# Kernel tuning notes

Measured on AMD Instinct MI355X. Metric: run time of the kernel, lower is better.

Reference implementation:

```python
import jax, jax.numpy as jnp
import numpy as np

B, T, C, H = 4, 1024, 1024, 16
D = C // H  # head dim = 64
EPS = 1e-5


def _layernorm(x, g, b):
    m = jnp.mean(x, axis=-1, keepdims=True)
    v = jnp.var(x, axis=-1, keepdims=True)
    return (x - m) / jnp.sqrt(v + EPS) * g + b


def setup_inputs() -> dict:
    key = jax.random.key(0)
    ks = jax.random.split(key, 8)
    s = 0.02  # GPT-style init scale
    w = lambda k, shp: (jax.random.normal(k, shp, jnp.float32) * s)
    return {
        "x": jax.random.normal(ks[0], (B, T, C), jnp.float32),
        "ln1_g": jnp.ones((C,), jnp.float32), "ln1_b": jnp.zeros((C,), jnp.float32),
        "wq": w(ks[1], (C, C)), "bq": jnp.zeros((C,), jnp.float32),
        "wk": w(ks[2], (C, C)), "bk": jnp.zeros((C,), jnp.float32),
        "wv": w(ks[3], (C, C)), "bv": jnp.zeros((C,), jnp.float32),
        "wo": w(ks[4], (C, C)), "bo": jnp.zeros((C,), jnp.float32),
        "ln2_g": jnp.ones((C,), jnp.float32), "ln2_b": jnp.zeros((C,), jnp.float32),
        "w1": w(ks[5], (C, 4 * C)), "b1": jnp.zeros((4 * C,), jnp.float32),
        "w2": w(ks[6], (4 * C, C)), "b2": jnp.zeros((C,), jnp.float32),
    }


def reference(x, ln1_g, ln1_b, wq, bq, wk, bk, wv, bv, wo, bo,
              ln2_g, ln2_b, w1, b1, w2, b2):
    # --- causal self-attention branch: x = x + attn(ln1(x)) ---
    h = _layernorm(x, ln1_g, ln1_b)
    q = (h @ wq + bq).reshape(B, T, H, D)
    k = (h @ wk + bk).reshape(B, T, H, D)
    v = (h @ wv + bv).reshape(B, T, H, D)
    att = jnp.einsum('bqhd,bkhd->bhqk', q, k) * (1.0 / np.sqrt(D).astype(np.float32))
    causal = jnp.tril(jnp.ones((T, T), bool))
    att = jnp.where(causal, att, -jnp.inf)
    att = jax.nn.softmax(att, axis=-1)  # dropout p=0 -> identity
    y = jnp.einsum('bhqk,bkhd->bqhd', att, v).reshape(B, T, C)
    x = x + (y @ wo + bo)
    # --- MLP branch: x = x + mlp(ln2(x)) ---
    h2 = _layernorm(x, ln2_g, ln2_b)
    m = jax.nn.gelu(h2 @ w1 + b1, approximate=False)  # torch nn.GELU default = exact erf
    x = x + (m @ w2 + b2)
    return x
```

## Files before the change

### kernel.cpp

```cpp
#include <hip/hip_runtime.h>
#include <hip/hip_bf16.h>
#include <math.h>

#define B_ 4
#define T_ 1024
#define C_ 1024
#define H_ 16
#define D_ 64
#define M_ (B_*T_)

typedef __bf16 bf16;
typedef __bf16 bf16x8 __attribute__((ext_vector_type(8)));
typedef float  f32x4  __attribute__((ext_vector_type(4)));

#define MFMA16(a, b, c) __builtin_amdgcn_mfma_f32_16x16x32_bf16((a), (b), (c), 0, 0, 0)

__device__ __forceinline__ void gload16(const void* g, void* l) {
  __builtin_amdgcn_global_load_lds((const __attribute__((address_space(1))) void*)g,
                                   (__attribute__((address_space(3))) void*)l,
                                   16, 0, 0);
}

__global__ __launch_bounds__(256) void wprep(const float* __restrict__ wq,
                                             const float* __restrict__ wk,
                                             const float* __restrict__ wv,
                                             const float* __restrict__ wo,
                                             const float* __restrict__ w1,
                                             const float* __restrict__ w2,
                                             bf16* __restrict__ WqkvT,
                                             bf16* __restrict__ WoT,
                                             bf16* __restrict__ W1T,
                                             bf16* __restrict__ W2T) {
  __shared__ float tile[32][33];
  const int b = blockIdx.x;
  const float* W; bf16* WT; int K, N, n0, k0;
  if (b < 3072)      { const int w = b >> 10, t = b & 1023;
                       W = (w == 0) ? wq : ((w == 1) ? wk : wv);
                       WT = WqkvT + (size_t)w * 1024 * 1024;
                       K = 1024; N = 1024; n0 = (t & 31) * 32; k0 = (t >> 5) * 32; }
  else if (b < 4096) { const int t = b - 3072; W = wo; WT = WoT;
                       K = 1024; N = 1024; n0 = (t & 31) * 32; k0 = (t >> 5) * 32; }
  else if (b < 8192) { const int t = b - 4096; W = w1; WT = W1T;
                       K = 1024; N = 4096; n0 = (t & 127) * 32; k0 = (t >> 7) * 32; }
  else               { const int t = b - 8192; W = w2; WT = W2T;
                       K = 4096; N = 1024; n0 = (t & 31) * 32; k0 = (t >> 5) * 32; }
  const int tx = threadIdx.x & 31, ty = threadIdx.x >> 5;
#pragma unroll
  for (int i = ty; i < 32; i += 8)
    tile[i][tx] = W[(size_t)(k0 + i) * N + n0 + tx];
  __syncthreads();
#pragma unroll
  for (int i = ty; i < 32; i += 8)
    WT[(size_t)(n0 + i) * K + k0 + tx] = (bf16)tile[tx][i];
}

__global__ __launch_bounds__(256) void bcat(const float* __restrict__ a,
                                            const float* __restrict__ b,
                                            const float* __restrict__ c,
                                            float* __restrict__ o) {
  int i = blockIdx.x * 256 + threadIdx.x;
  o[i] = (i < 1024) ? a[i] : ((i < 2048) ? b[i - 1024] : c[i - 2048]);
}

__global__ __launch_bounds__(256) void ln_k(const float* __restrict__ x,
                                            const float* __restrict__ g,
                                            const float* __restrict__ b,
                                            bf16* __restrict__ out) {
  int row = blockIdx.x;
  int t = threadIdx.x;
  float4 xv = ((const float4*)(x + (size_t)row * C_))[t];
  float s  = xv.x + xv.y + xv.z + xv.w;
  float ss = xv.x*xv.x + xv.y*xv.y + xv.z*xv.z + xv.w*xv.w;
#pragma unroll
  for (int m = 32; m; m >>= 1) { s += __shfl_xor(s, m); ss += __shfl_xor(ss, m); }
  __shared__ float red[8];
  int wid = t >> 6;
  if ((t & 63) == 0) { red[wid] = s; red[4 + wid] = ss; }
  __syncthreads();
  s  = red[0] + red[1] + red[2] + red[3];
  ss = red[4] + red[5] + red[6] + red[7];
  float mean = s * (1.0f / C_);
  float var  = ss * (1.0f / C_) - mean * mean;
  float inv  = rsqrtf(var + 1e-5f);
  float4 gv = ((const float4*)g)[t];
  float4 bv = ((const float4*)b)[t];
  bf16* o = out + (size_t)row * C_ + t * 4;
  o[0] = (bf16)((xv.x - mean) * inv * gv.x + bv.x);
  o[1] = (bf16)((xv.y - mean) * inv * gv.y + bv.y);
  o[2] = (bf16)((xv.z - mean) * inv * gv.z + bv.z);
  o[3] = (bf16)((xv.w - mean) * inv * gv.w + bv.w);
}

template <int BM, int BN, int WM, int WN, int EPI>
__global__ __launch_bounds__(WM*WN*64, 4)
void gemms(const bf16* __restrict__ A, const bf16* __restrict__ BT,
           const float* __restrict__ bias, const float* __restrict__ res,
           void* __restrict__ outp, int N, int K, int gx) {
  constexpr int NT = WM * WN * 64;
  constexpr int FM = BM / WM / 16, FN = BN / WN / 16;
  constexpr int RA = BM / 32, RB = BN / 32;
  __shared__ __align__(16) bf16 smem[(BM + BN) * 64];
  bf16* sA = smem;
  bf16* sB = smem + BM * 64;
  const int tid = threadIdx.x, lane = tid & 63, wid = tid >> 6;
  const int wr = wid / WN, wc = wid % WN;

  int bid = blockIdx.x;
  const int nwg = gridDim.x;
  if (!(nwg & 7)) bid = (bid & 7) * (nwg >> 3) + (bid >> 3);
  const int bx = bid % gx, by = bid / gx;
  const size_t am0 = (size_t)bx * BM, bn0 = (size_t)by * BN;

  f32x4 acc[FM][FN];
  const f32x4 fz = {0.f, 0.f, 0.f, 0.f};
#pragma unroll
  for (int m = 0; m < FM; ++m)
#pragma unroll
    for (int n = 0; n < FN; ++n) acc[m][n] = fz;

  const int srow = tid >> 3;
  const int sg = (tid & 7) ^ (srow & 7);
  const bf16* ag = A  + (am0 + srow) * (size_t)K + sg * 8;
  const bf16* bg = BT + (bn0 + srow) * (size_t)K + sg * 8;

  const int arow = lane & 15;
  const int g0 = (((lane >> 4))     ^ (lane & 7)) * 8;
  const int g1 = (((lane >> 4) + 4) ^ (lane & 7)) * 8;
  const int nt = K >> 6;

#pragma unroll
  for (int r = 0; r < RA; ++r)
    gload16(ag + (size_t)(r * 32) * K, sA + r * 2048 + tid * 8);
#pragma unroll
  for (int r = 0; r < RB; ++r)
    gload16(bg + (size_t)(r * 32) * K, sB + r * 2048 + tid * 8);

  for (int t = 0; t < nt; ++t) {
    __syncthreads();

    const bf16* pa = sA + (wr * (BM / WM) + arow) * 64;
    const bf16* pb = sB + (wc * (BN / WN) + arow) * 64;
    bf16x8 a[FM], b[FN];
#pragma unroll
    for (int m = 0; m < FM; ++m) a[m] = *(const bf16x8*)(pa + m * 16 * 64 + g0);
#pragma unroll
    for (int n = 0; n < FN; ++n) b[n] = *(const bf16x8*)(pb + n * 16 * 64 + g0);
#pragma unroll
    for (int m = 0; m < FM; ++m)
#pragma unroll
      for (int n = 0; n < FN; ++n)
        acc[m][n] = MFMA16(a[m], b[n], acc[m][n]);
    bf16x8 a1[FM], b1[FN];
#pragma unroll
    for (int m = 0; m < FM; ++m) a1[m] = *(const bf16x8*)(pa + m * 16 * 64 + g1);
#pragma unroll
    for (int n = 0; n < FN; ++n) b1[n] = *(const bf16x8*)(pb + n * 16 * 64 + g1);

    __syncthreads();

    if (t + 1 < nt) {
#pragma unroll
      for (int r = 0; r < RA; ++r)
        gload16(ag + (size_t)(t + 1) * 64 + (size_t)(r * 32) * K,
                sA + r * 2048 + tid * 8);
#pragma unroll
      for (int r = 0; r < RB; ++r)
        gload16(bg + (size_t)(t + 1) * 64 + (size_t)(r * 32) * K,
                sB + r * 2048 + tid * 8);
    }
#pragma unroll
    for (int m = 0; m < FM; ++m)
#pragma unroll
      for (int n = 0; n < FN; ++n)
        acc[m][n] = MFMA16(a1[m], b1[n], acc[m][n]);
  }

  if constexpr (EPI != 2) {
#pragma unroll
    for (int m = 0; m < FM; ++m) {
      const int row0 = wr * (BM / WM) + m * 16 + (lane >> 4) * 4;
#pragma unroll
      for (int n = 0; n < FN; ++n) {
        const int col = wc * (BN / WN) + n * 16 + (lane & 15);
        const float bv = bias[bn0 + col];
#pragma unroll
        for (int j = 0; j < 4; ++j) {
          float v = acc[m][n][j] + bv;
          if constexpr (EPI == 1) v = 0.5f * v * (1.0f + erff(v * 0.70710678118f));
          const int rr = row0 + j;
          smem[rr * BN + (((col >> 3) ^ (rr & 7)) << 3) + (col & 7)] = (bf16)v;
        }
      }
    }
    __syncthreads();
    constexpr int GR = BN / 8;
    constexpr int SI = BM * BN / (NT * 8);
#pragma unroll
    for (int i = 0; i < SI; ++i) {
      const int idx = i * NT + tid;
      const int row = idx / GR, g = idx % GR;
      *(bf16x8*)((bf16*)outp + (am0 + row) * N + bn0 + g * 8) =
          *(const bf16x8*)(smem + row * BN + ((g ^ (row & 7)) << 3));
    }
  } else {
    constexpr int PR = BM / WM;
    float* sf = (float*)smem;
#pragma unroll
    for (int h = 0; h < WM; ++h) {
      __syncthreads();
      if (wr == h) {
#pragma unroll
        for (int m = 0; m < FM; ++m) {
          const int lr0 = m * 16 + (lane >> 4) * 4;
#pragma unroll
          for (int n = 0; n < FN; ++n) {
            const int col = wc * (BN / WN) + n * 16 + (lane & 15);
            const float bv = bias[bn0 + col];
#pragma unroll
            for (int j = 0; j < 4; ++j)
              sf[(lr0 + j) * BN + col] = acc[m][n][j] + bv;
          }
        }
      }
      __syncthreads();
      constexpr int SI = PR * BN / (NT * 4);
#pragma unroll
      for (int i = 0; i < SI; ++i) {
        const int flat = (i * NT + tid) * 4;
        const int row = flat / BN, c = flat % BN;
        const size_t gi = (am0 + h * PR + row) * N + bn0 + c;
        float4 rv = *(const float4*)(res + gi);
        float4 sv = *(const float4*)(sf + row * BN + c);
        rv.x += sv.x; rv.y += sv.y; rv.z += sv.z; rv.w += sv.w;
        *(float4*)((float*)outp + gi) = rv;
      }
    }
  }
}

__global__ __launch_bounds__(256) void attn_k(const bf16* __restrict__ Q,
                                              const bf16* __restrict__ Kb,
                                              const bf16* __restrict__ Vb,
                                              bf16* __restrict__ Y, int ld) {
  int bh = blockIdx.x;
  int b = bh >> 4, h = bh & 15;
  int qt = (int)gridDim.y - 1 - (int)blockIdx.y;
  int q0 = qt * 64;
  int tid = threadIdx.x, wid = tid >> 6, lane = tid & 63;

  __shared__ __align__(16) bf16 sK[2][64 * 64];
  __shared__ __align__(16) bf16 sVT[2][64 * 64];
  __shared__ __align__(16) bf16 sP[4][16 * 64];

  const size_t rowQ = (size_t)(b * T_ + q0 + wid * 16 + (lane & 15)) * ld + h * 64 + (lane >> 4) * 8;
  bf16x8 qf0 = *(const bf16x8*)(Q + rowQ);
  bf16x8 qf1 = *(const bf16x8*)(Q + rowQ + 32);

  float m_run[4] = {-1e30f, -1e30f, -1e30f, -1e30f};
  float l_run[4] = {0.f, 0.f, 0.f, 0.f};
  const f32x4 fz = {0.f, 0.f, 0.f, 0.f};
  f32x4 o[4];
#pragma unroll
  for (int i = 0; i < 4; ++i) o[i] = fz;

  const int kgr = (lane & 7) ^ (lane >> 3);
  const bf16* kg = Kb + (size_t)(b * T_ + wid * 16 + (lane >> 3)) * ld + h * 64 + kgr * 8;
  const int lkoff = (wid * 16) * 64;
  const bf16* vg = Vb + (size_t)(b * T_ + lane) * ld + h * 64;

  const int g0 = (((lane >> 4))     ^ (lane & 7)) * 8;
  const int g1 = (((lane >> 4) + 4) ^ (lane & 7)) * 8;

  gload16(kg,                   sK[0] + lkoff);
  gload16(kg + (size_t)8 * ld,  sK[0] + lkoff + 8 * 64);
  {
    bf16x8 v0 = *(const bf16x8*)(vg + wid * 8);
    bf16x8 v1 = *(const bf16x8*)(vg + (wid + 4) * 8);
#pragma unroll
    for (int j = 0; j < 8; ++j) {
      const int pc = ((((lane >> 3) ^ j) << 3) | (lane & 7));
      sVT[0][(wid * 8 + j) * 64 + pc]       = v0[j];
      sVT[0][((wid + 4) * 8 + j) * 64 + pc] = v1[j];
    }
  }

  for (int kt = 0; kt <= qt; ++kt) {
    const int cur = kt & 1, nxt = cur ^ 1;
    const bool pf = (kt < qt);
    __syncthreads();

    bf16x8 vn0, vn1;
    if (pf) {
      const size_t k1 = (size_t)(kt + 1) * 64;
      gload16(kg + k1 * ld,        sK[nxt] + lkoff);
      gload16(kg + (k1 + 8) * ld,  sK[nxt] + lkoff + 8 * 64);
      vn0 = *(const bf16x8*)(vg + k1 * ld + wid * 8);
      vn1 = *(const bf16x8*)(vg + k1 * ld + (wid + 4) * 8);
    }

    const int k0 = kt * 64;
    f32x4 s[4];
#pragma unroll
    for (int ni = 0; ni < 4; ++ni) {
      const bf16* kr = sK[cur] + (ni * 16 + (lane & 15)) * 64;
      bf16x8 kf0 = *(const bf16x8*)(kr + g0);
      bf16x8 kf1 = *(const bf16x8*)(kr + g1);
      f32x4 t = fz;
      t = MFMA16(qf0, kf0, t);
      t = MFMA16(qf1, kf1, t);
      s[ni] = t;
    }

    int rbase = q0 + wid * 16 + (lane >> 4) * 4;
    int cbase = k0 + (lane & 15);
    float tm[4] = {-1e30f, -1e30f, -1e30f, -1e30f};
#pragma unroll
    for (int ni = 0; ni < 4; ++ni)
#pragma unroll
      for (int j = 0; j < 4; ++j) {
        float v = s[ni][j] * 0.125f;
        if (cbase + ni * 16 > rbase + j) v = -1e30f;
        s[ni][j] = v;
        tm[j] = fmaxf(tm[j], v);
      }
#pragma unroll
    for (int j = 0; j < 4; ++j)
#pragma unroll
      for (int mk = 1; mk < 16; mk <<= 1)
        tm[j] = fmaxf(tm[j], __shfl_xor(tm[j], mk));

    float fac[4], rs[4] = {0.f, 0.f, 0.f, 0.f};
#pragma unroll
    for (int j = 0; j < 4; ++j) {
      float mn = fmaxf(m_run[j], tm[j]);
      fac[j] = __expf(m_run[j] - mn);
      m_run[j] = mn;
    }
#pragma unroll
    for (int ni = 0; ni < 4; ++ni)
#pragma unroll
      for (int j = 0; j < 4; ++j) {
        float p = __expf(s[ni][j] - m_run[j]);
        rs[j] += p;
        const int crow = (lane >> 4) * 4 + j;
        const int cg = (ni * 2 + ((lane & 15) >> 3)) ^ (crow & 7);
        sP[wid][crow * 64 + (cg << 3) + (lane & 7)] = (bf16)p;
      }
#pragma unroll
    for (int j = 0; j < 4; ++j) {
#pragma unroll
      for (int mk = 1; mk < 16; mk <<= 1)
        rs[j] += __shfl_xor(rs[j], mk);
      l_run[j] = l_run[j] * fac[j] + rs[j];
    }
#pragma unroll
    for (int df = 0; df < 4; ++df)
#pragma unroll
      for (int j = 0; j < 4; ++j)
        o[df][j] *= fac[j];

#pragma unroll
    for (int kk = 0; kk < 2; ++kk) {
      const int gk = kk ? g1 : g0;
      bf16x8 pf8 = *(const bf16x8*)(sP[wid] + (lane & 15) * 64 + gk);
#pragma unroll
      for (int df = 0; df < 4; ++df) {
        bf16x8 vf = *(const bf16x8*)(sVT[cur] + (df * 16 + (lane & 15)) * 64 + gk);
        o[df] = MFMA16(pf8, vf, o[df]);
      }
    }

    if (pf) {
#pragma unroll
      for (int j = 0; j < 8; ++j) {
        const int pc = ((((lane >> 3) ^ j) << 3) | (lane & 7));
        sVT[nxt][(wid * 8 + j) * 64 + pc]       = vn0[j];
        sVT[nxt][((wid + 4) * 8 + j) * 64 + pc] = vn1[j];
      }
    }
  }

#pragma unroll
  for (int df = 0; df < 4; ++df)
#pragma unroll
    for (int j = 0; j < 4; ++j) {
      int row = q0 + wid * 16 + (lane >> 4) * 4 + j;
      int d = df * 16 + (lane & 15);
      Y[(size_t)(b * T_ + row) * C_ + h * 64 + d] = (bf16)(o[df][j] / l_run[j]);
    }
}

extern "C" void kernel_launch(void* const* d_in, const int* in_sizes, int n_in,
                              void* d_out, int out_size, void* d_ws, size_t ws_size,
                              hipStream_t stream) {
  (void)in_sizes; (void)n_in; (void)out_size; (void)ws_size;
  const float* x    = (const float*)d_in[0];
  const float* ln1g = (const float*)d_in[1];
  const float* ln1b = (const float*)d_in[2];
  const float* wq   = (const float*)d_in[3];
  const float* bq   = (const float*)d_in[4];
  const float* wk   = (const float*)d_in[5];
  const float* bk   = (const float*)d_in[6];
  const float* wv   = (const float*)d_in[7];
  const float* bv   = (const float*)d_in[8];
  const float* wo   = (const float*)d_in[9];
  const float* bo   = (const float*)d_in[10];
  const float* ln2g = (const float*)d_in[11];
  const float* ln2b = (const float*)d_in[12];
  const float* w1   = (const float*)d_in[13];
  const float* b1   = (const float*)d_in[14];
  const float* w2   = (const float*)d_in[15];
  const float* b2   = (const float*)d_in[16];

  char* ws = (char*)d_ws;
  const size_t MB = 1024 * 1024;
  bf16* WqkvT = (bf16*)(ws +  0 * MB);
  bf16* WoT   = (bf16*)(ws +  6 * MB);
  bf16* W1T   = (bf16*)(ws +  8 * MB);
  bf16* W2T   = (bf16*)(ws + 16 * MB);
  bf16* hbuf  = (bf16*)(ws + 24 * MB);
  bf16* qkv   = (bf16*)(ws + 32 * MB);
  bf16* yb    = (bf16*)(ws + 56 * MB);
  bf16* mb    = (bf16*)(ws + 32 * MB);
  float* x1   = (float*)(ws + 64 * MB);
  float* bqkv = (float*)d_out;

  dim3 blk(256);
  wprep<<<12288, blk, 0, stream>>>(wq, wk, wv, wo, w1, w2, WqkvT, WoT, W1T, W2T);
  bcat<<<12, blk, 0, stream>>>(bq, bk, bv, bqkv);

  ln_k<<<M_, blk, 0, stream>>>(x, ln1g, ln1b, hbuf);
  gemms<128,128,2,2,0><<<768,  blk, 0, stream>>>(hbuf, WqkvT, bqkv, nullptr, qkv, 3072, 1024, 32);
  attn_k<<<dim3(64, 16), blk, 0, stream>>>(qkv, qkv + 1024, qkv + 2048, yb, 3072);
  gemms<64,128,2,2,2><<<512,   blk, 0, stream>>>(yb, WoT, bo, x, x1, 1024, 1024, 64);
  ln_k<<<M_, blk, 0, stream>>>(x1, ln2g, ln2b, hbuf);
  gemms<128,128,2,2,1><<<1024, blk, 0, stream>>>(hbuf, W1T, b1, nullptr, mb, 4096, 1024, 32);
  gemms<64,128,2,2,2><<<512,   blk, 0, stream>>>(mb, W2T, b2, x1, (float*)d_out, 1024, 4096, 64);
}
```

Measured before the change: 218.2 us.

## Fuse prep kernels and process two query tiles per attention block

Merges the weight transpose/convert, bias concat and first layernorm into one launch, and switches the transpose to 64x64 tiles with vectorized float4 loads and bf16x8 stores. The attention kernel now handles 128 query rows per block as two 64-row subtiles that share each loaded K/V tile, halving K/V traffic and the grid size. It also adds a launch-bounds occupancy hint. In exchange, each attention thread holds more registers and the grid has fewer blocks, which can reduce parallelism and worsen causal load balance.

```diff
diff --git a/kernel.cpp b/kernel.cpp
--- a/kernel.cpp
+++ b/kernel.cpp
@@ -21,45 +21,75 @@
                                    16, 0, 0);
 }
 
-__global__ __launch_bounds__(256) void wprep(const float* __restrict__ wq,
-                                             const float* __restrict__ wk,
-                                             const float* __restrict__ wv,
-                                             const float* __restrict__ wo,
-                                             const float* __restrict__ w1,
-                                             const float* __restrict__ w2,
-                                             bf16* __restrict__ WqkvT,
-                                             bf16* __restrict__ WoT,
-                                             bf16* __restrict__ W1T,
-                                             bf16* __restrict__ W2T) {
-  __shared__ float tile[32][33];
-  const int b = blockIdx.x;
-  const float* W; bf16* WT; int K, N, n0, k0;
-  if (b < 3072)      { const int w = b >> 10, t = b & 1023;
-                       W = (w == 0) ? wq : ((w == 1) ? wk : wv);
-                       WT = WqkvT + (size_t)w * 1024 * 1024;
-                       K = 1024; N = 1024; n0 = (t & 31) * 32; k0 = (t >> 5) * 32; }
-  else if (b < 4096) { const int t = b - 3072; W = wo; WT = WoT;
-                       K = 1024; N = 1024; n0 = (t & 31) * 32; k0 = (t >> 5) * 32; }
-  else if (b < 8192) { const int t = b - 4096; W = w1; WT = W1T;
-                       K = 1024; N = 4096; n0 = (t & 127) * 32; k0 = (t >> 7) * 32; }
-  else               { const int t = b - 8192; W = w2; WT = W2T;
-                       K = 4096; N = 1024; n0 = (t & 31) * 32; k0 = (t >> 5) * 32; }
-  const int tx = threadIdx.x & 31, ty = threadIdx.x >> 5;
-#pragma unroll
-  for (int i = ty; i < 32; i += 8)
-    tile[i][tx] = W[(size_t)(k0 + i) * N + n0 + tx];
-  __syncthreads();
-#pragma unroll
-  for (int i = ty; i < 32; i += 8)
-    WT[(size_t)(n0 + i) * K + k0 + tx] = (bf16)tile[tx][i];
-}
-
-__global__ __launch_bounds__(256) void bcat(const float* __restrict__ a,
-                                            const float* __restrict__ b,
-                                            const float* __restrict__ c,
-                                            float* __restrict__ o) {
-  int i = blockIdx.x * 256 + threadIdx.x;
-  o[i] = (i < 1024) ? a[i] : ((i < 2048) ? b[i - 1024] : c[i - 2048]);
+__global__ __launch_bounds__(256) void prep_k(
+    const float* __restrict__ x, const float* __restrict__ ln1g,
+    const float* __restrict__ ln1b,
+    const float* __restrict__ wq, const float* __restrict__ wk,
+    const float* __restrict__ wv, const float* __restrict__ wo,
+    const float* __restrict__ w1, const float* __restrict__ w2,
+    const float* __restrict__ bq, const float* __restrict__ bk,
+    const float* __restrict__ bv,
+    bf16* __restrict__ WqkvT, bf16* __restrict__ WoT,
+    bf16* __restrict__ W1T, bf16* __restrict__ W2T,
+    bf16* __restrict__ hbuf, float* __restrict__ bqkv) {
+  __shared__ float tile[64][65];
+  const int blk = blockIdx.x, tid = threadIdx.x;
+  if (blk < 3072) {
+    const float* W; bf16* WT; int K, N, n0, k0;
+    if (blk < 1024)      { const int w = blk >> 8, t = blk & 255;
+                           W  = (w == 0) ? wq : (w == 1) ? wk : (w == 2) ? wv : wo;
+                           WT = (w < 3) ? WqkvT + (size_t)w * 1024 * 1024 : WoT;
+                           K = 1024; N = 1024; n0 = (t & 15) * 64; k0 = (t >> 4) * 64; }
+    else if (blk < 2048) { const int t = blk - 1024; W = w1; WT = W1T;
+                           K = 1024; N = 4096; n0 = (t & 63) * 64; k0 = (t >> 6) * 64; }
+    else                 { const int t = blk - 2048; W = w2; WT = W2T;
+                           K = 4096; N = 1024; n0 = (t & 15) * 64; k0 = (t >> 4) * 64; }
+    const int tr = tid >> 4, tc4 = (tid & 15) * 4;
+#pragma unroll
+    for (int p = 0; p < 4; ++p) {
+      float4 v = *(const float4*)(W + (size_t)(k0 + tr + p * 16) * N + n0 + tc4);
+      tile[tr + p * 16][tc4]     = v.x;
+      tile[tr + p * 16][tc4 + 1] = v.y;
+      tile[tr + p * 16][tc4 + 2] = v.z;
+      tile[tr + p * 16][tc4 + 3] = v.w;
+    }
+    __syncthreads();
+    const int nr = tid >> 3, k8 = (tid & 7) * 8;
+#pragma unroll
+    for (int p = 0; p < 2; ++p) {
+      const int n = nr + p * 32;
+      bf16x8 o8;
+#pragma unroll
+      for (int j = 0; j < 8; ++j) o8[j] = (bf16)tile[k8 + j][n];
+      *(bf16x8*)(WT + (size_t)(n0 + n) * K + k0 + k8) = o8;
+    }
+  } else if (blk < 7168) {
+    const int row = blk - 3072;
+    float4 xv = ((const float4*)(x + (size_t)row * C_))[tid];
+    float s  = xv.x + xv.y + xv.z + xv.w;
+    float ss = xv.x*xv.x + xv.y*xv.y + xv.z*xv.z + xv.w*xv.w;
+#pragma unroll
+    for (int m = 32; m; m >>= 1) { s += __shfl_xor(s, m); ss += __shfl_xor(ss, m); }
+    float* red = &tile[0][0];
+    const int wid = tid >> 6;
+    if ((tid & 63) == 0) { red[wid] = s; red[4 + wid] = ss; }
+    __syncthreads();
+    s  = red[0] + red[1] + red[2] + red[3];
+    ss = red[4] + red[5] + red[6] + red[7];
+    const float mean = s * (1.0f / C_);
+    const float var  = ss * (1.0f / C_) - mean * mean;
+    const float inv  = rsqrtf(var + 1e-5f);
+    float4 gv = ((const float4*)ln1g)[tid];
+    float4 bv = ((const float4*)ln1b)[tid];
+    bf16* o = hbuf + (size_t)row * C_ + tid * 4;
+    o[0] = (bf16)((xv.x - mean) * inv * gv.x + bv.x);
+    o[1] = (bf16)((xv.y - mean) * inv * gv.y + bv.y);
+    o[2] = (bf16)((xv.z - mean) * inv * gv.z + bv.z);
+    o[3] = (bf16)((xv.w - mean) * inv * gv.w + bv.w);
+  } else {
+    const int i = (blk - 7168) * 256 + tid;
+    bqkv[i] = (i < 1024) ? bq[i] : ((i < 2048) ? bk[i - 1024] : bv[i - 2048]);
+  }
 }
 
 __global__ __launch_bounds__(256) void ln_k(const float* __restrict__ x,
@@ -238,30 +268,33 @@
   }
 }
 
-__global__ __launch_bounds__(256) void attn_k(const bf16* __restrict__ Q,
-                                              const bf16* __restrict__ Kb,
-                                              const bf16* __restrict__ Vb,
-                                              bf16* __restrict__ Y, int ld) {
-  int bh = blockIdx.x;
-  int b = bh >> 4, h = bh & 15;
-  int qt = (int)gridDim.y - 1 - (int)blockIdx.y;
-  int q0 = qt * 64;
-  int tid = threadIdx.x, wid = tid >> 6, lane = tid & 63;
+__global__ __launch_bounds__(256, 4) void attn_k(const bf16* __restrict__ Q,
+                                                 const bf16* __restrict__ Kb,
+                                                 const bf16* __restrict__ Vb,
+                                                 bf16* __restrict__ Y, int ld) {
+  const int bh = blockIdx.x;
+  const int b = bh >> 4, h = bh & 15;
+  const int u = (int)gridDim.y - 1 - (int)blockIdx.y;
+  const int q0 = u * 128;
+  const int tid = threadIdx.x, wid = tid >> 6, lane = tid & 63;
 
   __shared__ __align__(16) bf16 sK[2][64 * 64];
   __shared__ __align__(16) bf16 sVT[2][64 * 64];
   __shared__ __align__(16) bf16 sP[4][16 * 64];
 
-  const size_t rowQ = (size_t)(b * T_ + q0 + wid * 16 + (lane & 15)) * ld + h * 64 + (lane >> 4) * 8;
-  bf16x8 qf0 = *(const bf16x8*)(Q + rowQ);
-  bf16x8 qf1 = *(const bf16x8*)(Q + rowQ + 32);
-
-  float m_run[4] = {-1e30f, -1e30f, -1e30f, -1e30f};
-  float l_run[4] = {0.f, 0.f, 0.f, 0.f};
+  const size_t rowQ0 = (size_t)(b * T_ + q0 + wid * 16 + (lane & 15)) * ld + h * 64 + (lane >> 4) * 8;
+  const bf16x8 qaf0 = *(const bf16x8*)(Q + rowQ0);
+  const bf16x8 qaf1 = *(const bf16x8*)(Q + rowQ0 + 32);
+  const size_t rowQ1 = rowQ0 + (size_t)64 * ld;
+  const bf16x8 qbf0 = *(const bf16x8*)(Q + rowQ1);
+  const bf16x8 qbf1 = *(const bf16x8*)(Q + rowQ1 + 32);
+
   const f32x4 fz = {0.f, 0.f, 0.f, 0.f};
-  f32x4 o[4];
-#pragma unroll
-  for (int i = 0; i < 4; ++i) o[i] = fz;
+  float mA[4] = {-1e30f, -1e30f, -1e30f, -1e30f}, lA[4] = {0.f, 0.f, 0.f, 0.f};
+  float mB[4] = {-1e30f, -1e30f, -1e30f, -1e30f}, lB[4] = {0.f, 0.f, 0.f, 0.f};
+  f32x4 oA[4], oB[4];
+#pragma unroll
+  for (int i = 0; i < 4; ++i) { oA[i] = fz; oB[i] = fz; }
 
   const int kgr = (lane & 7) ^ (lane >> 3);
   const bf16* kg = Kb + (size_t)(b * T_ + wid * 16 + (lane >> 3)) * ld + h * 64 + kgr * 8;
@@ -284,21 +317,11 @@
     }
   }
 
-  for (int kt = 0; kt <= qt; ++kt) {
-    const int cur = kt & 1, nxt = cur ^ 1;
-    const bool pf = (kt < qt);
-    __syncthreads();
-
-    bf16x8 vn0, vn1;
-    if (pf) {
-      const size_t k1 = (size_t)(kt + 1) * 64;
-      gload16(kg + k1 * ld,        sK[nxt] + lkoff);
-      gload16(kg + (k1 + 8) * ld,  sK[nxt] + lkoff + 8 * 64);
-      vn0 = *(const bf16x8*)(vg + k1 * ld + wid * 8);
-      vn1 = *(const bf16x8*)(vg + k1 * ld + (wid + 4) * 8);
-    }
-
-    const int k0 = kt * 64;
+  const int ktmax = 2 * u + 1;
+  int k0 = 0, cur = 0;
+
+  auto subtile = [&](const bf16x8& qf0, const bf16x8& qf1, int rbase,
+                     float* m_run, float* l_run, f32x4* o) {
     f32x4 s[4];
 #pragma unroll
     for (int ni = 0; ni < 4; ++ni) {
@@ -310,9 +333,7 @@
       t = MFMA16(qf1, kf1, t);
       s[ni] = t;
     }
-
-    int rbase = q0 + wid * 16 + (lane >> 4) * 4;
-    int cbase = k0 + (lane & 15);
+    const int cbase = k0 + (lane & 15);
     float tm[4] = {-1e30f, -1e30f, -1e30f, -1e30f};
 #pragma unroll
     for (int ni = 0; ni < 4; ++ni)
@@ -358,7 +379,6 @@
 #pragma unroll
       for (int j = 0; j < 4; ++j)
         o[df][j] *= fac[j];
-
 #pragma unroll
     for (int kk = 0; kk < 2; ++kk) {
       const int gk = kk ? g1 : g0;
@@ -369,6 +389,28 @@
         o[df] = MFMA16(pf8, vf, o[df]);
       }
     }
+  };
+
+  for (int kt = 0; kt <= ktmax; ++kt) {
+    cur = kt & 1;
+    const int nxt = cur ^ 1;
+    const bool pf = (kt < ktmax);
+    __syncthreads();
+
+    bf16x8 vn0, vn1;
+    if (pf) {
+      const size_t k1 = (size_t)(kt + 1) * 64;
+      gload16(kg + k1 * ld,        sK[nxt] + lkoff);
+      gload16(kg + (k1 + 8) * ld,  sK[nxt] + lkoff + 8 * 64);
+      vn0 = *(const bf16x8*)(vg + k1 * ld + wid * 8);
+      vn1 = *(const bf16x8*)(vg + k1 * ld + (wid + 4) * 8);
+    }
+
+    k0 = kt * 64;
+    const int rb = q0 + wid * 16 + (lane >> 4) * 4;
+    if (kt < ktmax)
+      subtile(qaf0, qaf1, rb,      mA, lA, oA);
+    subtile(qbf0, qbf1, rb + 64,   mB, lB, oB);
 
     if (pf) {
 #pragma unroll
@@ -384,9 +426,10 @@
   for (int df = 0; df < 4; ++df)
 #pragma unroll
     for (int j = 0; j < 4; ++j) {
-      int row = q0 + wid * 16 + (lane >> 4) * 4 + j;
-      int d = df * 16 + (lane & 15);
-      Y[(size_t)(b * T_ + row) * C_ + h * 64 + d] = (bf16)(o[df][j] / l_run[j]);
+      const int row = q0 + wid * 16 + (lane >> 4) * 4 + j;
+      const int d = df * 16 + (lane & 15);
+      Y[(size_t)(b * T_ + row) * C_ + h * 64 + d]      = (bf16)(oA[df][j] / lA[j]);
+      Y[(size_t)(b * T_ + row + 64) * C_ + h * 64 + d] = (bf16)(oB[df][j] / lB[j]);
     }
 }
 
@@ -426,12 +469,10 @@
   float* bqkv = (float*)d_out;
 
   dim3 blk(256);
-  wprep<<<12288, blk, 0, stream>>>(wq, wk, wv, wo, w1, w2, WqkvT, WoT, W1T, W2T);
-  bcat<<<12, blk, 0, stream>>>(bq, bk, bv, bqkv);
-
-  ln_k<<<M_, blk, 0, stream>>>(x, ln1g, ln1b, hbuf);
+  prep_k<<<7180, blk, 0, stream>>>(x, ln1g, ln1b, wq, wk, wv, wo, w1, w2,
+                                   bq, bk, bv, WqkvT, WoT, W1T, W2T, hbuf, bqkv);
   gemms<128,128,2,2,0><<<768,  blk, 0, stream>>>(hbuf, WqkvT, bqkv, nullptr, qkv, 3072, 1024, 32);
-  attn_k<<<dim3(64, 16), blk, 0, stream>>>(qkv, qkv + 1024, qkv + 2048, yb, 3072);
+  attn_k<<<dim3(64, 8), blk, 0, stream>>>(qkv, qkv + 1024, qkv + 2048, yb, 3072);
   gemms<64,128,2,2,2><<<512,   blk, 0, stream>>>(yb, WoT, bo, x, x1, 1024, 1024, 64);
   ln_k<<<M_, blk, 0, stream>>>(x1, ln2g, ln2b, hbuf);
   gemms<128,128,2,2,1><<<1024, blk, 0, stream>>>(hbuf, W1T, b1, nullptr, mb, 4096, 1024, 32);
```

Result: slower. 261.5 us (+19.9%).
